# Kernel tuning notes

Measured on AMD Instinct MI355X. Metric: run time of the kernel, lower is better.

Reference implementation:

```python
import jax, jax.numpy as jnp
import numpy as np
from jax.ops import segment_sum, segment_max

N = 38332
E = 1200000
C = 64
POI_LEN = 38333
CAT_LEN = 400
LAYERS = 5


def _glorot(key, shape):
    fan_in, fan_out = shape[0], shape[-1]
    lim = float(np.sqrt(6.0 / (fan_in + fan_out)))
    return jax.random.uniform(key, shape, jnp.float32, -lim, lim)


def gcn_conv(x, src, dst, ew, W, b):
    # PyG GCNConv: x@W, add self-loops (weight 1), symmetric norm, scatter-sum at dst
    h = x @ W  # [N, Cout]
    ar = jnp.arange(N, dtype=src.dtype)
    s = jnp.concatenate([src, ar])
    d = jnp.concatenate([dst, ar])
    w = jnp.concatenate([ew, jnp.ones((N,), ew.dtype)])
    deg = segment_sum(w, d, num_segments=N)
    dinv = jnp.where(deg > 0, jax.lax.rsqrt(jnp.maximum(deg, 1e-12)), 0.0)
    norm = dinv[s] * w * dinv[d]
    out = segment_sum(h[s] * norm[:, None], d, num_segments=N)
    return out + b


def graph_norm(x, w, b, alpha, eps=1e-5):
    mean = jnp.mean(x, axis=0, keepdims=True)
    out = x - alpha * mean
    var = jnp.mean(out * out, axis=0, keepdims=True)
    return out * jax.lax.rsqrt(var + eps) * w + b


def gat_conv(x, src, dst, W, att_src, att_dst, b):
    # PyG GATConv, heads=1, add_self_loops=True, negative_slope=0.2
    h = x @ W  # [N, C]
    ar = jnp.arange(N, dtype=src.dtype)
    s = jnp.concatenate([src, ar])
    d = jnp.concatenate([dst, ar])
    a_s = h @ att_src  # [N]
    a_d = h @ att_dst
    e = jax.nn.leaky_relu(a_s[s] + a_d[d], 0.2)  # [E+N]
    m = segment_max(e, d, num_segments=N)
    ex = jnp.exp(e - m[d])
    z = segment_sum(ex, d, num_segments=N)
    alpha = ex / (z[d] + 1e-16)
    out = segment_sum(h[s] * alpha[:, None], d, num_segments=N)
    return out + b


def setup_inputs() -> dict:
    key = jax.random.key(0)
    ks = jax.random.split(key, 32)
    inp = {
        'poi_idx': jax.random.randint(ks[0], (N,), 0, POI_LEN, jnp.int32),
        'cat_idx': jax.random.randint(ks[1], (N,), 0, CAT_LEN, jnp.int32),
        'feat': jax.random.normal(ks[2], (N, 3), jnp.float32),
        'edge_index': jax.random.randint(ks[3], (2, E), 0, N, jnp.int32),
        'weight': jax.random.uniform(ks[4], (E,), jnp.float32),
        'poi_emb': jax.random.normal(ks[5], (POI_LEN, 300), jnp.float32),
        'cat_emb': jax.random.normal(ks[6], (CAT_LEN, 100), jnp.float32),
        'W_in': _glorot(ks[7], (403, C)),
        'b_in': jnp.zeros((C,), jnp.float32),
        'gcn_W': jax.vmap(lambda k: _glorot(k, (C, C)))(jax.random.split(ks[8], LAYERS)),
        'gcn_b': jnp.zeros((LAYERS, C), jnp.float32),
        'gn_w': jnp.ones((LAYERS, C), jnp.float32),
        'gn_b': jnp.zeros((LAYERS, C), jnp.float32),
        'gn_a': jnp.ones((LAYERS, C), jnp.float32),
        'gat_W': jax.vmap(lambda k: _glorot(k, (C, C)))(jax.random.split(ks[9], LAYERS)),
        'gat_att_src': jax.random.normal(ks[10], (LAYERS, C), jnp.float32) * 0.1,
        'gat_att_dst': jax.random.normal(ks[11], (LAYERS, C), jnp.float32) * 0.1,
        'gat_b': jnp.zeros((LAYERS, C), jnp.float32),
        'W_out': _glorot(ks[12], (C, 1)),
        'b_out': jnp.zeros((1,), jnp.float32),
        'fc1_W': _glorot(ks[13], (N, 128)),
        'fc1_b': jnp.zeros((128,), jnp.float32),
        'fc2_W': _glorot(ks[14], (128, POI_LEN)),
        'fc2_b': jnp.zeros((POI_LEN,), jnp.float32),
    }
    return inp


def reference(poi_idx, cat_idx, feat, edge_index, weight, poi_emb, cat_emb,
              W_in, b_in, gcn_W, gcn_b, gn_w, gn_b, gn_a,
              gat_W, gat_att_src, gat_att_dst, gat_b,
              W_out, b_out, fc1_W, fc1_b, fc2_W, fc2_b):
    src, dst = edge_index[0], edge_index[1]
    lrelu = lambda v: jax.nn.leaky_relu(v, 0.01)  # nn.LeakyReLU default
    x = jnp.concatenate([poi_emb[poi_idx], cat_emb[cat_idx], feat], axis=1)  # [N,403]
    x = lrelu(gcn_conv(x, src, dst, weight, W_in, b_in))  # [N,64]
    for i in range(LAYERS):
        t = gcn_conv(x, src, dst, weight, gcn_W[i], gcn_b[i])
        t = lrelu(graph_norm(t, gn_w[i], gn_b[i], gn_a[i]))
        x = x + t
        t = gat_conv(x, src, dst, gat_W[i], gat_att_src[i], gat_att_dst[i], gat_b[i])
        t = lrelu(graph_norm(t, gn_w[i], gn_b[i], gn_a[i]))
        x = x + t
    x = lrelu(gcn_conv(x, src, dst, weight, W_out, b_out)).reshape(-1)  # [N]
    h = jax.nn.relu(x @ fc1_W + fc1_b)
    out = jax.nn.relu(h @ fc2_W + fc2_b)  # [POI_LEN]
    return out
```

## Files before the change

### kernel.cpp

```cpp
#include <hip/hip_runtime.h>
#include <hip/hip_fp16.h>

#define NN 38332
#define NE 1200000
#define POI 38333
#define NWG 128
#define CHUNK (NE/NWG)
#define SBLK 256

__device__ __forceinline__ float lrelu01(float v){ return v > 0.f ? v : 0.01f*v; }

__device__ __forceinline__ void load8(const __half* h, int s, int c8, float* f){
  uint4 q = *(const uint4*)((const __half*)h + (size_t)s*64 + c8);
  __half2 h0 = *(__half2*)&q.x, h1 = *(__half2*)&q.y, h2 = *(__half2*)&q.z, h3 = *(__half2*)&q.w;
  float2 r0 = __half22float2(h0), r1 = __half22float2(h1), r2 = __half22float2(h2), r3 = __half22float2(h3);
  f[0]=r0.x; f[1]=r0.y; f[2]=r1.x; f[3]=r1.y; f[4]=r2.x; f[5]=r2.y; f[6]=r3.x; f[7]=r3.y;
}
__device__ __forceinline__ void load8(const float* h, int s, int c8, float* f){
  float4 a = *(const float4*)(h + (size_t)s*64 + c8);
  float4 b = *(const float4*)(h + (size_t)s*64 + c8 + 4);
  f[0]=a.x; f[1]=a.y; f[2]=a.z; f[3]=a.w; f[4]=b.x; f[5]=b.y; f[6]=b.z; f[7]=b.w;
}
__device__ __forceinline__ void store8(float* out, int n, int cb, const float* o){
  *(float4*)&out[(size_t)n*64 + cb]     = make_float4(o[0],o[1],o[2],o[3]);
  *(float4*)&out[(size_t)n*64 + cb + 4] = make_float4(o[4],o[5],o[6],o[7]);
}
__device__ __forceinline__ void store8(__half* out, int n, int cb, const float* o){
  __half2 q0 = __floats2half2_rn(o[0], o[1]);
  __half2 q1 = __floats2half2_rn(o[2], o[3]);
  __half2 q2 = __floats2half2_rn(o[4], o[5]);
  __half2 q3 = __floats2half2_rn(o[6], o[7]);
  uint4 q;
  q.x = *(unsigned*)&q0; q.y = *(unsigned*)&q1; q.z = *(unsigned*)&q2; q.w = *(unsigned*)&q3;
  *(uint4*)((__half*)out + (size_t)n*64 + cb) = q;
}

__global__ __launch_bounds__(1024) void k_hist(const int* __restrict__ dst,
                                               int* __restrict__ partial){
  __shared__ int hist[NN];
  for (int i = threadIdx.x; i < NN; i += 1024) hist[i] = 0;
  __syncthreads();
  int base = blockIdx.x*CHUNK;
  for (int k = threadIdx.x; k < CHUNK; k += 1024)
    atomicAdd(&hist[dst[base + k]], 1);
  __syncthreads();
  for (int i = threadIdx.x; i < NN; i += 1024)
    partial[(size_t)blockIdx.x*NN + i] = hist[i];
}

__global__ __launch_bounds__(256) void k_b1(int* __restrict__ partial, int* __restrict__ counts){
  int bin = blockIdx.x*256 + threadIdx.x;
  if (bin < NN){
    int run = 0;
    for (int wg = 0; wg < NWG; ++wg){
      int v = partial[(size_t)wg*NN + bin];
      partial[(size_t)wg*NN + bin] = run;
      run += v;
    }
    counts[bin] = run;
  }
}

__global__ __launch_bounds__(1024) void k_scan(const int* __restrict__ counts, int* rowptr){
  __shared__ int part[1024];
  int tid = threadIdx.x;
  const int per = (NN + 1023)/1024;
  int base = tid*per;
  int s = 0;
  for (int k = 0; k < per; k++){ int i = base + k; if (i < NN) s += counts[i]; }
  part[tid] = s;
  __syncthreads();
  for (int off = 1; off < 1024; off <<= 1){
    int v = (tid >= off) ? part[tid-off] : 0;
    __syncthreads();
    part[tid] += v;
    __syncthreads();
  }
  int run = (tid == 0) ? 0 : part[tid-1];
  for (int k = 0; k < per; k++){
    int i = base + k;
    if (i < NN){ rowptr[i] = run; run += counts[i]; }
  }
  if (tid == 1023) rowptr[NN] = run;
}

__global__ __launch_bounds__(1024) void k_scatter(const int* __restrict__ src,
                                                  const int* __restrict__ dst,
                                                  const float* __restrict__ ew,
                                                  const int* __restrict__ rowptr,
                                                  const int* __restrict__ partial,
                                                  int2* __restrict__ cw){
  __shared__ int cur[NN];
  for (int i = threadIdx.x; i < NN; i += 1024)
    cur[i] = rowptr[i] + partial[(size_t)blockIdx.x*NN + i];
  __syncthreads();
  int base = blockIdx.x*CHUNK;
  for (int k = threadIdx.x; k < CHUNK; k += 1024){
    int e = base + k;
    int d = dst[e];
    int pos = atomicAdd(&cur[d], 1);
    cw[pos] = make_int2(src[e], __float_as_int(ew[e]));
  }
}

__global__ __launch_bounds__(256) void k_dinv(const int* __restrict__ rowptr,
                                              const int2* __restrict__ cw,
                                              float* __restrict__ dinv){
  int lane = threadIdx.x & 63;
  int n = blockIdx.x*4 + (threadIdx.x >> 6);
  int beg = rowptr[n], end = rowptr[n+1];
  float s = 0.f;
  for (int e = beg + lane; e < end; e += 64) s += __int_as_float(cw[e].y);
  #pragma unroll
  for (int off = 32; off; off >>= 1) s += __shfl_xor(s, off);
  if (lane == 0) dinv[n] = rsqrtf(1.0f + s);
}

__global__ __launch_bounds__(256) void k_scale(const int* __restrict__ rowptr,
                                               const float* __restrict__ dinv,
                                               int2* __restrict__ cw){
  int lane = threadIdx.x & 63;
  int n = blockIdx.x*4 + (threadIdx.x >> 6);
  float dn = dinv[n];
  int beg = rowptr[n], end = rowptr[n+1];
  for (int e = beg + lane; e < end; e += 64){
    int2 p = cw[e];
    cw[e].y = __float_as_int(dinv[p.x]*__int_as_float(p.y)*dn);
  }
}

template<int KC, int KS>
__global__ __launch_bounds__(256) void k_proj(const float* __restrict__ emb,
                                              const float* __restrict__ W,
                                              float* __restrict__ outp, int rows){
  int lane = threadIdx.x & 63;
  int base = __builtin_amdgcn_readfirstlane(blockIdx.x*32 + (threadIdx.x >> 6)*8);
  float acc[8] = {0.f,0.f,0.f,0.f,0.f,0.f,0.f,0.f};
  constexpr int NCH = (KC + 63)/64;
  #pragma unroll
  for (int ch = 0; ch < NCH; ++ch){
    float Wreg[64];
    #pragma unroll
    for (int j = 0; j < 64; ++j)
      Wreg[j] = (ch*64 + j < KC) ? W[(ch*64 + j)*64 + lane] : 0.f;
    #pragma unroll
    for (int r = 0; r < 8; ++r){
      int row = base + r;
      if (row < rows){
        const float* er = emb + (size_t)row*KS + ch*64;
        #pragma unroll
        for (int j = 0; j < 64; ++j)
          if (ch*64 + j < KC) acc[r] = fmaf(er[j], Wreg[j], acc[r]);
      }
    }
  }
  #pragma unroll
  for (int r = 0; r < 8; ++r){
    int row = base + r;
    if (row < rows) outp[(size_t)row*64 + lane] = acc[r];
  }
}

__global__ __launch_bounds__(256) void k_gather(const int* __restrict__ poi_idx,
                                                const int* __restrict__ cat_idx,
                                                const float* __restrict__ feat,
                                                const float* __restrict__ pp1,
                                                const float* __restrict__ pp2,
                                                const float* __restrict__ cproj,
                                                const float* __restrict__ Wf,
                                                float* __restrict__ outh){
  int i = blockIdx.x*256 + threadIdx.x;
  int n = i >> 6, c = i & 63;
  int pi = poi_idx[n];
  float f0 = feat[n*3], f1 = feat[n*3+1], f2 = feat[n*3+2];
  float v = pp1[(size_t)pi*64 + c] + pp2[(size_t)pi*64 + c] + cproj[(size_t)cat_idx[n]*64 + c];
  v = fmaf(f0, Wf[c], v);
  v = fmaf(f1, Wf[64 + c], v);
  v = fmaf(f2, Wf[128 + c], v);
  outh[i] = v;
}

template<bool ATT, bool RESID>
__global__ __launch_bounds__(256) void k_lin64f(float* __restrict__ x,
                                                const __half* __restrict__ t,
                                                const float* __restrict__ stats,
                                                const float* __restrict__ gb,
                                                const float* __restrict__ W,
                                                const float* __restrict__ att_src,
                                                const float* __restrict__ att_dst,
                                                __half* __restrict__ h,
                                                float* __restrict__ a_s,
                                                float* __restrict__ a_d){
  int lane = threadIdx.x & 63;
  int base = blockIdx.x*32 + (threadIdx.x >> 6)*8;
  float Wreg[64];
  #pragma unroll
  for (int j = 0; j < 64; ++j) Wreg[j] = W[j*64 + lane];
  float coef = 0.f, shift = 0.f, gbv = 0.f;
  if (RESID){
    coef  = stats[128 + lane];
    shift = stats[192 + lane];
    gbv   = gb[lane];
  }
  float as_l = 0.f, ad_l = 0.f;
  if (ATT){ as_l = att_src[lane]; ad_l = att_dst[lane]; }
  #pragma unroll
  for (int r = 0; r < 8; ++r){
    int row = base + r;
    if (row < NN){
      float xn = x[(size_t)row*64 + lane];
      if (RESID){
        float tv = __half2float(t[(size_t)row*64 + lane]);
        xn += lrelu01((tv - shift)*coef + gbv);
        x[(size_t)row*64 + lane] = xn;
      }
      int xi = __float_as_int(xn);
      float acc = 0.f;
      #pragma unroll
      for (int j = 0; j < 64; ++j)
        acc = fmaf(__int_as_float(__builtin_amdgcn_readlane(xi, j)), Wreg[j], acc);
      h[(size_t)row*64 + lane] = __float2half(acc);
      if (ATT){
        float s1 = acc*as_l, s2 = acc*ad_l;
        #pragma unroll
        for (int off = 32; off; off >>= 1){ s1 += __shfl_xor(s1, off); s2 += __shfl_xor(s2, off); }
        if (lane == 0){ a_s[row] = s1; a_d[row] = s2; }
      }
    }
  }
}

template<bool DO_LRELU, typename TIN, typename TOUT>
__global__ __launch_bounds__(256) void k_gcn_prop(const TIN* __restrict__ h,
                                                  const int* __restrict__ rowptr,
                                                  const int2* __restrict__ cw,
                                                  const float* __restrict__ dinv,
                                                  const float* __restrict__ bias,
                                                  TOUT* __restrict__ out){
  int lane = threadIdx.x & 63;
  int n = __builtin_amdgcn_readfirstlane(blockIdx.x*4 + (threadIdx.x >> 6));
  int beg = rowptr[n], end = rowptr[n+1];
  int deg = end - beg;
  int g  = lane >> 3;
  int c8 = (lane & 7) << 3;
  float acc[8] = {0.f,0.f,0.f,0.f,0.f,0.f,0.f,0.f};
  if (deg < 64){
    int sv = n; float wv = 0.f;
    if (lane < deg){
      int2 p = cw[beg + lane];
      sv = p.x; wv = __int_as_float(p.y);
    } else if (lane == deg){
      float di = dinv[n];
      wv = di*di;
    }
    int ne = deg + 1;
    int nit = (ne + 7) >> 3;
    float w0 = __shfl(wv, g);
    int  sj0 = __shfl(sv, g);
    float f0[8]; load8(h, sj0, c8, f0);
    for (int it = 1; it < nit; ++it){
      int ei = (it << 3) + g;
      float w1 = __shfl(wv, ei);
      int  sj1 = __shfl(sv, ei);
      float f1[8]; load8(h, sj1, c8, f1);
      #pragma unroll
      for (int j = 0; j < 8; ++j) acc[j] = fmaf(w0, f0[j], acc[j]);
      w0 = w1;
      #pragma unroll
      for (int j = 0; j < 8; ++j) f0[j] = f1[j];
    }
    #pragma unroll
    for (int j = 0; j < 8; ++j) acc[j] = fmaf(w0, f0[j], acc[j]);
  } else {
    {
      float di = dinv[n];
      float w = (g == 0) ? di*di : 0.f;
      float f[8]; load8(h, n, c8, f);
      #pragma unroll
      for (int j = 0; j < 8; ++j) acc[j] = fmaf(w, f[j], acc[j]);
    }
    int nit = (deg + 7) >> 3;
    for (int it = 0; it < nit; ++it){
      int ei = (it << 3) + g;
      int2 p = cw[beg + (ei < deg ? ei : 0)];
      float w = (ei < deg) ? __int_as_float(p.y) : 0.f;
      float f[8]; load8(h, p.x, c8, f);
      #pragma unroll
      for (int j = 0; j < 8; ++j) acc[j] = fmaf(w, f[j], acc[j]);
    }
  }
  #pragma unroll
  for (int m = 8; m < 64; m <<= 1){
    #pragma unroll
    for (int j = 0; j < 8; ++j) acc[j] += __shfl_xor(acc[j], m);
  }
  if (lane < 8){
    int cb = lane << 3;
    float4 b0 = *(const float4*)&bias[cb];
    float4 b1 = *(const float4*)&bias[cb + 4];
    float o[8] = {acc[0]+b0.x, acc[1]+b0.y, acc[2]+b0.z, acc[3]+b0.w,
                  acc[4]+b1.x, acc[5]+b1.y, acc[6]+b1.z, acc[7]+b1.w};
    if (DO_LRELU){
      #pragma unroll
      for (int j = 0; j < 8; ++j) o[j] = lrelu01(o[j]);
    }
    store8(out, n, cb, o);
  }
}

__global__ __launch_bounds__(256) void k_gat_prop(const __half* __restrict__ h,
                                                  const int* __restrict__ rowptr,
                                                  const int2* __restrict__ cw,
                                                  const float* __restrict__ a_s,
                                                  const float* __restrict__ a_d,
                                                  const float* __restrict__ bias,
                                                  __half* __restrict__ out){
  int lane = threadIdx.x & 63;
  int n = __builtin_amdgcn_readfirstlane(blockIdx.x*4 + (threadIdx.x >> 6));
  int beg = rowptr[n], end = rowptr[n+1];
  int deg = end - beg;
  float ad = a_d[n];
  float se = a_s[n] + ad; se = se > 0.f ? se : 0.2f*se;
  if (deg <= 64){
    int s = 0; float v = -1e30f;
    if (lane < deg){
      s = cw[beg + lane].x;
      v = a_s[s] + ad; v = v > 0.f ? v : 0.2f*v;
    }
    float m = fmaxf(se, v);
    #pragma unroll
    for (int off = 32; off; off >>= 1) m = fmaxf(m, __shfl_xor(m, off));
    float ev = (lane < deg) ? __expf(v - m) : 0.f;
    float z = ev;
    #pragma unroll
    for (int off = 32; off; off >>= 1) z += __shfl_xor(z, off);
    float es = __expf(se - m);
    z += es;
    float zinv = 1.0f/(z + 1e-16f);
    int g = lane >> 3, c8 = (lane & 7) << 3;
    float acc[8] = {0.f,0.f,0.f,0.f,0.f,0.f,0.f,0.f};
    { float f[8]; load8(h, n, c8, f);
      float w = (g == 0) ? es : 0.f;
      #pragma unroll
      for (int j = 0; j < 8; ++j) acc[j] = fmaf(w, f[j], acc[j]);
    }
    int nit = (deg + 7) >> 3;
    if (nit > 0){
      float w0 = __shfl(ev, g);
      int  sj0 = __shfl(s,  g);
      float f0[8]; load8(h, sj0, c8, f0);
      for (int it = 1; it < nit; ++it){
        int ei = (it << 3) + g;
        float w1 = __shfl(ev, ei);
        int  sj1 = __shfl(s,  ei);
        float f1[8]; load8(h, sj1, c8, f1);
        #pragma unroll
        for (int j = 0; j < 8; ++j) acc[j] = fmaf(w0, f0[j], acc[j]);
        w0 = w1;
        #pragma unroll
        for (int j = 0; j < 8; ++j) f0[j] = f1[j];
      }
      #pragma unroll
      for (int j = 0; j < 8; ++j) acc[j] = fmaf(w0, f0[j], acc[j]);
    }
    #pragma unroll
    for (int mm = 8; mm < 64; mm <<= 1){
      #pragma unroll
      for (int j = 0; j < 8; ++j) acc[j] += __shfl_xor(acc[j], mm);
    }
    if (lane < 8){
      int cb = lane << 3;
      float4 b0 = *(const float4*)&bias[cb];
      float4 b1 = *(const float4*)&bias[cb + 4];
      float o[8] = {fmaf(acc[0],zinv,b0.x), fmaf(acc[1],zinv,b0.y), fmaf(acc[2],zinv,b0.z), fmaf(acc[3],zinv,b0.w),
                    fmaf(acc[4],zinv,b1.x), fmaf(acc[5],zinv,b1.y), fmaf(acc[6],zinv,b1.z), fmaf(acc[7],zinv,b1.w)};
      store8(out, n, cb, o);
    }
  } else {
    float m = se;
    for (int e = beg + lane; e < end; e += 64){
      float v = a_s[cw[e].x] + ad; v = v > 0.f ? v : 0.2f*v;
      m = fmaxf(m, v);
    }
    #pragma unroll
    for (int off = 32; off; off >>= 1) m = fmaxf(m, __shfl_xor(m, off));
    float z = 0.f;
    for (int e = beg + lane; e < end; e += 64){
      float v = a_s[cw[e].x] + ad; v = v > 0.f ? v : 0.2f*v;
      z += __expf(v - m);
    }
    #pragma unroll
    for (int off = 32; off; off >>= 1) z += __shfl_xor(z, off);
    float es = __expf(se - m);
    z += es;
    float zinv = 1.0f/(z + 1e-16f);
    float acc = es*(float)h[(size_t)n*64 + lane];
    for (int e = beg; e < end; ++e){
      int sj = cw[e].x;
      float v = a_s[sj] + ad; v = v > 0.f ? v : 0.2f*v;
      acc = fmaf(__expf(v - m), (float)h[(size_t)sj*64 + lane], acc);
    }
    out[(size_t)n*64 + lane] = __float2half(acc*zinv + bias[lane]);
  }
}

__global__ __launch_bounds__(256) void k_colstats(const __half* __restrict__ t,
                                                  float* __restrict__ pstats){
  int lane = threadIdx.x & 63;
  int sub  = threadIdx.x >> 6;
  float s = 0.f, s2 = 0.f;
  for (int n = blockIdx.x*4 + sub; n < NN; n += gridDim.x*4){
    float v = __half2float(t[(size_t)n*64 + lane]);
    s += v; s2 = fmaf(v, v, s2);
  }
  __shared__ float ls[256], ls2[256];
  ls[threadIdx.x] = s; ls2[threadIdx.x] = s2;
  __syncthreads();
  if (threadIdx.x < 64){
    s  = ls[threadIdx.x]  + ls[threadIdx.x+64]  + ls[threadIdx.x+128]  + ls[threadIdx.x+192];
    s2 = ls2[threadIdx.x] + ls2[threadIdx.x+64] + ls2[threadIdx.x+128] + ls2[threadIdx.x+192];
    pstats[blockIdx.x*128 + threadIdx.x]      = s;
    pstats[blockIdx.x*128 + 64 + threadIdx.x] = s2;
  }
}

__global__ __launch_bounds__(256) void k_chan(const float* __restrict__ pstats,
                                              const float* __restrict__ gw,
                                              const float* __restrict__ ga,
                                              float* __restrict__ stats){
  int lane = threadIdx.x & 63, w = threadIdx.x >> 6;
  float s = 0.f, s2 = 0.f;
  for (int blk = w*(SBLK/4); blk < (w+1)*(SBLK/4); ++blk){
    s  += pstats[blk*128 + lane];
    s2 += pstats[blk*128 + 64 + lane];
  }
  __shared__ float ls[256], ls2[256];
  ls[threadIdx.x] = s; ls2[threadIdx.x] = s2;
  __syncthreads();
  if (threadIdx.x < 64){
    int c = threadIdx.x;
    s  = ls[c]  + ls[c+64]  + ls[c+128]  + ls[c+192];
    s2 = ls2[c] + ls2[c+64] + ls2[c+128] + ls2[c+192];
    const float invN = 1.0f/(float)NN;
    float m  = s*invN, ms = s2*invN, a = ga[c];
    float var = ms - m*m*a*(2.0f - a);
    stats[128 + c] = rsqrtf(var + 1e-5f)*gw[c];
    stats[192 + c] = a*m;
  }
}

__global__ __launch_bounds__(256) void k_outlinf(const float* __restrict__ x,
                                                 const __half* __restrict__ t,
                                                 const float* __restrict__ stats,
                                                 const float* __restrict__ gb,
                                                 const float* __restrict__ Wout,
                                                 float* __restrict__ h1){
  int lane = threadIdx.x & 63, wave = threadIdx.x >> 6;
  int n = blockIdx.x*4 + wave;
  float coef  = stats[128 + lane];
  float shift = stats[192 + lane];
  float xn = x[(size_t)n*64 + lane];
  float tv = __half2float(t[(size_t)n*64 + lane]);
  xn += lrelu01((tv - shift)*coef + gb[lane]);
  float v = xn*Wout[lane];
  #pragma unroll
  for (int off = 32; off; off >>= 1) v += __shfl_xor(v, off);
  if (lane == 0) h1[n] = v;
}

__global__ __launch_bounds__(256) void k_prop1(const float* __restrict__ h1,
                                               const int* __restrict__ rowptr,
                                               const int2* __restrict__ cw,
                                               const float* __restrict__ dinv,
                                               const float* __restrict__ b_out,
                                               float* __restrict__ xs){
  int lane = threadIdx.x & 63;
  int n = blockIdx.x*32 + (threadIdx.x >> 6)*8 + (lane >> 3);
  bool ok = n < NN;
  int beg = ok ? rowptr[n] : 0;
  int end = ok ? rowptr[n+1] : 0;
  float acc = 0.f;
  for (int e = beg + (lane & 7); e < end; e += 8){
    int2 p = cw[e];
    acc = fmaf(__int_as_float(p.y), h1[p.x], acc);
  }
  acc += __shfl_xor(acc, 1);
  acc += __shfl_xor(acc, 2);
  acc += __shfl_xor(acc, 4);
  if (ok && (lane & 7) == 0){
    float di = dinv[n];
    xs[n] = lrelu01(acc + di*di*h1[n] + b_out[0]);
  }
}

__global__ __launch_bounds__(256) void k_fc1(const float* __restrict__ xs,
                                             const float* __restrict__ W,
                                             float* __restrict__ pfc){
  int j = threadIdx.x & 127, half = threadIdx.x >> 7;
  float acc = 0.f;
  for (int n = blockIdx.x*2 + half; n < NN; n += gridDim.x*2)
    acc = fmaf(xs[n], W[(size_t)n*128 + j], acc);
  __shared__ float ls[256];
  ls[threadIdx.x] = acc;
  __syncthreads();
  if (threadIdx.x < 128) pfc[blockIdx.x*128 + j] = ls[j] + ls[128 + j];
}

__global__ __launch_bounds__(256) void k_fc2(const float* __restrict__ pfc,
                                             const float* __restrict__ fc1_b,
                                             const float* __restrict__ W2,
                                             const float* __restrict__ b2,
                                             float* __restrict__ out){
  __shared__ float hs[128];
  if (threadIdx.x < 128){
    float v = fc1_b[threadIdx.x];
    for (int blk = 0; blk < 128; ++blk) v += pfc[blk*128 + threadIdx.x];
    hs[threadIdx.x] = v > 0.f ? v : 0.f;
  }
  __syncthreads();
  int p = blockIdx.x*256 + threadIdx.x;
  if (p < POI){
    float acc = b2[p];
    #pragma unroll
    for (int j = 0; j < 128; j++) acc = fmaf(hs[j], W2[(size_t)j*POI + p], acc);
    out[p] = acc > 0.f ? acc : 0.f;
  }
}

extern "C" void kernel_launch(void* const* d_in, const int* in_sizes, int n_in,
                              void* d_out, int out_size, void* d_ws, size_t ws_size,
                              hipStream_t stream) {
  const int*   poi_idx = (const int*)d_in[0];
  const int*   cat_idx = (const int*)d_in[1];
  const float* feat    = (const float*)d_in[2];
  const int*   eidx    = (const int*)d_in[3];
  const int*   src     = eidx;
  const int*   dst     = eidx + NE;
  const float* ew      = (const float*)d_in[4];
  const float* poi_emb = (const float*)d_in[5];
  const float* cat_emb = (const float*)d_in[6];
  const float* W_in    = (const float*)d_in[7];
  const float* b_in    = (const float*)d_in[8];
  const float* gcn_W   = (const float*)d_in[9];
  const float* gcn_b   = (const float*)d_in[10];
  const float* gn_w    = (const float*)d_in[11];
  const float* gn_b    = (const float*)d_in[12];
  const float* gn_a    = (const float*)d_in[13];
  const float* gat_W   = (const float*)d_in[14];
  const float* att_s   = (const float*)d_in[15];
  const float* att_d   = (const float*)d_in[16];
  const float* gat_b   = (const float*)d_in[17];
  const float* W_out   = (const float*)d_in[18];
  const float* b_out   = (const float*)d_in[19];
  const float* fc1_W   = (const float*)d_in[20];
  const float* fc1_b   = (const float*)d_in[21];
  const float* fc2_W   = (const float*)d_in[22];
  const float* fc2_b   = (const float*)d_in[23];
  float* out = (float*)d_out;

  char* p = (char*)d_ws;
  auto alloc = [&](size_t bytes){ void* r = (void*)p; p += (bytes + 255) & ~(size_t)255; return r; };
  float*  x      = (float*) alloc((size_t)NN*64*4);
  float*  t32    = (float*) alloc((size_t)NN*64*4);
  __half* t      = (__half*)alloc((size_t)NN*64*2);
  __half* h      = (__half*)alloc((size_t)NN*64*2);
  int*    partial= (int*)   alloc((size_t)NWG*NN*4);
  float*  pproj1 = (float*) partial;
  float*  pproj2 = (float*) alloc((size_t)POI*64*4);
  float*  cproj  = (float*) alloc((size_t)400*64*4);
  int2*   cw     = (int2*)  alloc((size_t)NE*8);
  float*  dinv   = (float*) alloc(NN*4);
  int*    counts = (int*)   alloc(NN*4);
  int*    rowptr = (int*)   alloc((NN+1)*4);
  float*  a_s    = (float*) alloc(NN*4);
  float*  a_d    = (float*) alloc(NN*4);
  float*  pstats = (float*) alloc((size_t)SBLK*128*4);
  float*  stats  = (float*) alloc(256*4);
  float*  h1     = (float*) alloc(NN*4);
  float*  xs     = (float*) alloc(NN*4);
  float*  pfc    = (float*) alloc(128*128*4);

  const int G_N   = (NN + 255)/256;
  const int G_W4  = NN/4;
  const int G_L   = (NN + 31)/32;
  const int G_PJ  = (POI + 31)/32;
  const int G_EL  = NN*64/256;
  const int G_P1  = (NN + 31)/32;

  k_hist   <<<NWG, 1024, 0, stream>>>(dst, partial);
  k_b1     <<<G_N, 256, 0, stream>>>(partial, counts);
  k_scan   <<<1, 1024, 0, stream>>>(counts, rowptr);
  k_scatter<<<NWG, 1024, 0, stream>>>(src, dst, ew, rowptr, partial, cw);
  k_dinv   <<<G_W4, 256, 0, stream>>>(rowptr, cw, dinv);
  k_scale  <<<G_W4, 256, 0, stream>>>(rowptr, dinv, cw);

  k_proj<150,300><<<G_PJ, 256, 0, stream>>>(poi_emb,       W_in,          pproj1, POI);
  k_proj<150,300><<<G_PJ, 256, 0, stream>>>(poi_emb + 150, W_in + 150*64, pproj2, POI);
  k_proj<100,100><<<13, 256, 0, stream>>>(cat_emb, W_in + 300*64, cproj, 400);
  k_gather<<<G_EL, 256, 0, stream>>>(poi_idx, cat_idx, feat, pproj1, pproj2, cproj, W_in + 400*64, t32);
  k_gcn_prop<true, float, float><<<G_W4, 256, 0, stream>>>(t32, rowptr, cw, dinv, b_in, x);

  for (int i = 0; i < 5; i++){
    if (i == 0)
      k_lin64f<false,false><<<G_L, 256, 0, stream>>>(x, nullptr, nullptr, nullptr,
                                                     gcn_W, nullptr, nullptr, h, nullptr, nullptr);
    else
      k_lin64f<false,true><<<G_L, 256, 0, stream>>>(x, t, stats, gn_b + (i-1)*64,
                                                    gcn_W + i*4096, nullptr, nullptr, h, nullptr, nullptr);
    k_gcn_prop<false, __half, __half><<<G_W4, 256, 0, stream>>>(h, rowptr, cw, dinv, gcn_b + i*64, t);
    k_colstats<<<SBLK, 256, 0, stream>>>(t, pstats);
    k_chan<<<1, 256, 0, stream>>>(pstats, gn_w + i*64, gn_a + i*64, stats);
    k_lin64f<true,true><<<G_L, 256, 0, stream>>>(x, t, stats, gn_b + i*64,
                                                 gat_W + i*4096, att_s + i*64, att_d + i*64, h, a_s, a_d);
    k_gat_prop<<<G_W4, 256, 0, stream>>>(h, rowptr, cw, a_s, a_d, gat_b + i*64, t);
    k_colstats<<<SBLK, 256, 0, stream>>>(t, pstats);
    k_chan<<<1, 256, 0, stream>>>(pstats, gn_w + i*64, gn_a + i*64, stats);
  }

  k_outlinf<<<G_W4, 256, 0, stream>>>(x, t, stats, gn_b + 4*64, W_out, h1);
  k_prop1<<<G_P1, 256, 0, stream>>>(h1, rowptr, cw, dinv, b_out, xs);
  k_fc1<<<128, 256, 0, stream>>>(xs, fc1_W, pfc);
  k_fc2<<<(POI + 255)/256, 256, 0, stream>>>(pfc, fc1_b, fc2_W, fc2_b, out);
}
```

Measured before the change: 1.027 ms.

## Merge POI projection halves, widen fc1 grid, split fc2 reduction across lanes

The two half-width POI embedding projections become a single K=300 projection, which removes one launch and one intermediate buffer. The fc1 grid grows from 128 to 1024 blocks for more parallelism, and the partial-sum reduction moves into a separate single-block kernel. fc2 now splits each output's 128-term dot product across 4 lanes with shuffle reduction, so 4x more blocks can hide the latency of the strided weight reads. In exchange there is one extra launch, a larger partial buffer, and a K=300 projection that holds more weight chunks per thread.

```diff
diff --git a/kernel.cpp b/kernel.cpp
--- a/kernel.cpp
+++ b/kernel.cpp
@@ -7,6 +7,7 @@
 #define NWG 128
 #define CHUNK (NE/NWG)
 #define SBLK 256
+#define FBLK 1024
 
 __device__ __forceinline__ float lrelu01(float v){ return v > 0.f ? v : 0.01f*v; }
 
@@ -129,28 +130,28 @@
   }
 }
 
-template<int KC, int KS>
+template<int K>
 __global__ __launch_bounds__(256) void k_proj(const float* __restrict__ emb,
                                               const float* __restrict__ W,
                                               float* __restrict__ outp, int rows){
   int lane = threadIdx.x & 63;
   int base = __builtin_amdgcn_readfirstlane(blockIdx.x*32 + (threadIdx.x >> 6)*8);
   float acc[8] = {0.f,0.f,0.f,0.f,0.f,0.f,0.f,0.f};
-  constexpr int NCH = (KC + 63)/64;
+  constexpr int NCH = (K + 63)/64;
   #pragma unroll
   for (int ch = 0; ch < NCH; ++ch){
     float Wreg[64];
     #pragma unroll
     for (int j = 0; j < 64; ++j)
-      Wreg[j] = (ch*64 + j < KC) ? W[(ch*64 + j)*64 + lane] : 0.f;
+      Wreg[j] = (ch*64 + j < K) ? W[(ch*64 + j)*64 + lane] : 0.f;
     #pragma unroll
     for (int r = 0; r < 8; ++r){
       int row = base + r;
       if (row < rows){
-        const float* er = emb + (size_t)row*KS + ch*64;
+        const float* er = emb + (size_t)row*K + ch*64;
         #pragma unroll
         for (int j = 0; j < 64; ++j)
-          if (ch*64 + j < KC) acc[r] = fmaf(er[j], Wreg[j], acc[r]);
+          if (ch*64 + j < K) acc[r] = fmaf(er[j], Wreg[j], acc[r]);
       }
     }
   }
@@ -164,16 +165,14 @@
 __global__ __launch_bounds__(256) void k_gather(const int* __restrict__ poi_idx,
                                                 const int* __restrict__ cat_idx,
                                                 const float* __restrict__ feat,
-                                                const float* __restrict__ pp1,
-                                                const float* __restrict__ pp2,
+                                                const float* __restrict__ pproj,
                                                 const float* __restrict__ cproj,
                                                 const float* __restrict__ Wf,
                                                 float* __restrict__ outh){
   int i = blockIdx.x*256 + threadIdx.x;
   int n = i >> 6, c = i & 63;
-  int pi = poi_idx[n];
   float f0 = feat[n*3], f1 = feat[n*3+1], f2 = feat[n*3+2];
-  float v = pp1[(size_t)pi*64 + c] + pp2[(size_t)pi*64 + c] + cproj[(size_t)cat_idx[n]*64 + c];
+  float v = pproj[(size_t)poi_idx[n]*64 + c] + cproj[(size_t)cat_idx[n]*64 + c];
   v = fmaf(f0, Wf[c], v);
   v = fmaf(f1, Wf[64 + c], v);
   v = fmaf(f2, Wf[128 + c], v);
@@ -506,24 +505,42 @@
   if (threadIdx.x < 128) pfc[blockIdx.x*128 + j] = ls[j] + ls[128 + j];
 }
 
-__global__ __launch_bounds__(256) void k_fc2(const float* __restrict__ pfc,
+__global__ __launch_bounds__(256) void k_fcr(const float* __restrict__ pfc,
                                              const float* __restrict__ fc1_b,
+                                             float* __restrict__ hfc){
+  int j = threadIdx.x & 127, half = threadIdx.x >> 7;
+  float acc = 0.f;
+  for (int blk = half; blk < FBLK; blk += 2)
+    acc += pfc[blk*128 + j];
+  __shared__ float ls[256];
+  ls[threadIdx.x] = acc;
+  __syncthreads();
+  if (threadIdx.x < 128){
+    float v = ls[threadIdx.x] + ls[128 + threadIdx.x] + fc1_b[threadIdx.x];
+    hfc[threadIdx.x] = v > 0.f ? v : 0.f;
+  }
+}
+
+__global__ __launch_bounds__(256) void k_fc2(const float* __restrict__ hfc,
                                              const float* __restrict__ W2,
                                              const float* __restrict__ b2,
                                              float* __restrict__ out){
   __shared__ float hs[128];
-  if (threadIdx.x < 128){
-    float v = fc1_b[threadIdx.x];
-    for (int blk = 0; blk < 128; ++blk) v += pfc[blk*128 + threadIdx.x];
-    hs[threadIdx.x] = v > 0.f ? v : 0.f;
-  }
-  __syncthreads();
-  int p = blockIdx.x*256 + threadIdx.x;
+  if (threadIdx.x < 128) hs[threadIdx.x] = hfc[threadIdx.x];
+  __syncthreads();
+  int p = blockIdx.x*64 + (threadIdx.x >> 2);
+  int q = threadIdx.x & 3;
   if (p < POI){
-    float acc = b2[p];
-    #pragma unroll
-    for (int j = 0; j < 128; j++) acc = fmaf(hs[j], W2[(size_t)j*POI + p], acc);
-    out[p] = acc > 0.f ? acc : 0.f;
+    float acc = 0.f;
+    #pragma unroll
+    for (int j = q; j < 128; j += 4)
+      acc = fmaf(hs[j], W2[(size_t)j*POI + p], acc);
+    acc += __shfl_xor(acc, 1);
+    acc += __shfl_xor(acc, 2);
+    if (q == 0){
+      float v = acc + b2[p];
+      out[p] = v > 0.f ? v : 0.f;
+    }
   }
 }
 
@@ -565,8 +582,7 @@
   __half* t      = (__half*)alloc((size_t)NN*64*2);
   __half* h      = (__half*)alloc((size_t)NN*64*2);
   int*    partial= (int*)   alloc((size_t)NWG*NN*4);
-  float*  pproj1 = (float*) partial;
-  float*  pproj2 = (float*) alloc((size_t)POI*64*4);
+  float*  pproj  = (float*) partial;
   float*  cproj  = (float*) alloc((size_t)400*64*4);
   int2*   cw     = (int2*)  alloc((size_t)NE*8);
   float*  dinv   = (float*) alloc(NN*4);
@@ -578,7 +594,8 @@
   float*  stats  = (float*) alloc(256*4);
   float*  h1     = (float*) alloc(NN*4);
   float*  xs     = (float*) alloc(NN*4);
-  float*  pfc    = (float*) alloc(128*128*4);
+  float*  pfc    = (float*) alloc((size_t)FBLK*128*4);
+  float*  hfc    = (float*) alloc(128*4);
 
   const int G_N   = (NN + 255)/256;
   const int G_W4  = NN/4;
@@ -586,6 +603,7 @@
   const int G_PJ  = (POI + 31)/32;
   const int G_EL  = NN*64/256;
   const int G_P1  = (NN + 31)/32;
+  const int G_F2  = (POI + 63)/64;
 
   k_hist   <<<NWG, 1024, 0, stream>>>(dst, partial);
   k_b1     <<<G_N, 256, 0, stream>>>(partial, counts);
@@ -594,10 +612,9 @@
   k_dinv   <<<G_W4, 256, 0, stream>>>(rowptr, cw, dinv);
   k_scale  <<<G_W4, 256, 0, stream>>>(rowptr, dinv, cw);
 
-  k_proj<150,300><<<G_PJ, 256, 0, stream>>>(poi_emb,       W_in,          pproj1, POI);
-  k_proj<150,300><<<G_PJ, 256, 0, stream>>>(poi_emb + 150, W_in + 150*64, pproj2, POI);
-  k_proj<100,100><<<13, 256, 0, stream>>>(cat_emb, W_in + 300*64, cproj, 400);
-  k_gather<<<G_EL, 256, 0, stream>>>(poi_idx, cat_idx, feat, pproj1, pproj2, cproj, W_in + 400*64, t32);
+  k_proj<300><<<G_PJ, 256, 0, stream>>>(poi_emb, W_in, pproj, POI);
+  k_proj<100><<<13, 256, 0, stream>>>(cat_emb, W_in + 300*64, cproj, 400);
+  k_gather<<<G_EL, 256, 0, stream>>>(poi_idx, cat_idx, feat, pproj, cproj, W_in + 400*64, t32);
   k_gcn_prop<true, float, float><<<G_W4, 256, 0, stream>>>(t32, rowptr, cw, dinv, b_in, x);
 
   for (int i = 0; i < 5; i++){
@@ -619,6 +636,7 @@
 
   k_outlinf<<<G_W4, 256, 0, stream>>>(x, t, stats, gn_b + 4*64, W_out, h1);
   k_prop1<<<G_P1, 256, 0, stream>>>(h1, rowptr, cw, dinv, b_out, xs);
-  k_fc1<<<128, 256, 0, stream>>>(xs, fc1_W, pfc);
-  k_fc2<<<(POI + 255)/256, 256, 0, stream>>>(pfc, fc1_b, fc2_W, fc2_b, out);
-}
+  k_fc1<<<FBLK, 256, 0, stream>>>(xs, fc1_W, pfc);
+  k_fcr<<<1, 256, 0, stream>>>(pfc, fc1_b, hfc);
+  k_fc2<<<G_F2, 256, 0, stream>>>(hfc, fc2_W, fc2_b, out);
+}
```

Result: slower. 1.111 ms (+8.1%).
